# Kernel optimization log

Measured on AMD Instinct MI355X. Metric: run time of the kernel, lower is better.

## Reference

```python
import jax, jax.numpy as jnp
import numpy as np

DIM = 256
HID = 1024
BATCH = 16384
STEP_SIZE = 0.1
NSTEPS = 10  # int(1.0 / step_size)


def setup_inputs() -> dict:
    key = jax.random.key(0)
    ks = jax.random.split(key, 8)
    x = jax.random.normal(ks[0], (BATCH, DIM), dtype=jnp.float32)
    # Scaled init so tanh layers stay in a sane range (like default torch init).
    W1 = jax.random.normal(ks[1], (DIM + 1, HID), dtype=jnp.float32) / np.sqrt(DIM + 1)
    b1 = jnp.zeros((HID,), dtype=jnp.float32)
    W2 = jax.random.normal(ks[2], (HID, HID), dtype=jnp.float32) / np.sqrt(HID)
    b2 = jnp.zeros((HID,), dtype=jnp.float32)
    W3 = jax.random.normal(ks[3], (HID, DIM), dtype=jnp.float32) / np.sqrt(HID)
    b3 = jnp.zeros((DIM,), dtype=jnp.float32)
    proj_mat = jax.random.normal(ks[4], (DIM, DIM), dtype=jnp.float32)
    return {"x": x, "W1": W1, "b1": b1, "W2": W2, "b2": b2,
            "W3": W3, "b3": b3, "proj_mat": proj_mat}


def reference(x, W1, b1, W2, b2, W3, b3, proj_mat):
    """FlowProposal.log_prob: backward RK4 integration of dx/dt = v(x,t)
    from t=1 to t=0 with Hutchinson trace estimation via forward-mode JVP.
    Returns log q(x), shape [batch]."""
    dtype = x.dtype

    def net(xc, t):
        # VelocityMLP: concat(x, t) -> tanh MLP -> velocity [B, DIM]
        tcol = jnp.broadcast_to(jnp.asarray(t, dtype), (xc.shape[0], 1))
        h = jnp.tanh(jnp.concatenate([xc, tcol], axis=1) @ W1 + b1)
        h = jnp.tanh(h @ W2 + b2)
        return h @ W3 + b3

    # Deterministic hashed Hutchinson noise (from the INITIAL x, as in torch).
    noise = jnp.sin((x @ proj_mat) * 1000.0) * 1.41421356  # sqrt(2)

    def dyn(xc, t):
        v, jv = jax.jvp(lambda xi: net(xi, t), (xc,), (noise,))
        tr = jnp.sum(noise * jv, axis=1, keepdims=True)  # eps^T J eps, [B,1]
        return v, tr

    dt = -STEP_SIZE

    def step(carry, k):
        xt, ljt = carry
        t = 1.0 + dt * k
        v1, tr1 = dyn(xt, t)
        v2, tr2 = dyn(xt + dt * 0.5 * v1, t + dt * 0.5)
        v3, tr3 = dyn(xt + dt * 0.5 * v2, t + dt * 0.5)
        v4, tr4 = dyn(xt + dt * v3, t + dt)
        xt = xt + (dt / 6.0) * (v1 + 2 * v2 + 2 * v3 + v4)
        ljt = ljt + (dt / 6.0) * (tr1 + 2 * tr2 + 2 * tr3 + tr4)
        return (xt, ljt), None

    init = (x, jnp.zeros((x.shape[0], 1), dtype))
    (xt, ljt), _ = jax.lax.scan(step, init, jnp.arange(NSTEPS, dtype=dtype))

    log_prob_z = -0.5 * jnp.sum(xt * xt, axis=1) - 0.5 * DIM * jnp.log(jnp.asarray(2.0 * np.pi, dtype))
    return log_prob_z - ljt[:, 0]
```

## Files before the change

### kernel.cpp

```cpp
#include <hip/hip_runtime.h>
#include <stdint.h>
#include <stddef.h>

typedef unsigned short ushort_t;
typedef float f32x4 __attribute__((ext_vector_type(4)));
typedef short short8 __attribute__((ext_vector_type(8)));

#define NB 16384
#define DIMX 256
#define HIDX 1024
#define DTC (-0.1f)

__device__ __forceinline__ unsigned short f2bf_bits(float f){
  unsigned int u = __float_as_uint(f);
  unsigned int r = (u + 0x7FFFu + ((u >> 16) & 1u)) >> 16;
  return (unsigned short)r;
}
__device__ __forceinline__ float bf2f_bits(unsigned short s){
  return __uint_as_float(((unsigned int)s) << 16);
}
__device__ __forceinline__ float fast_tanh(float x){
  float a = fabsf(x);
  float e = __expf(a + a);
  float r = 1.0f - 2.0f / (e + 1.0f);
  return copysignf(r, x);
}
__device__ __forceinline__ void gload16(const void* g, void* l){
  __builtin_amdgcn_global_load_lds(
      (const __attribute__((address_space(1))) void*)g,
      (__attribute__((address_space(3))) void*)l, 16, 0, 0);
}
__device__ __forceinline__ int ldsx(int r, int c){
  return r * 64 + (c ^ ((r & 7) << 3));
}

__global__ void prep_weights(const float* __restrict__ W1, const float* __restrict__ W2,
                             const float* __restrict__ W3,
                             ushort_t* __restrict__ W1at, ushort_t* __restrict__ W2t,
                             ushort_t* __restrict__ W3t){
  int i = blockIdx.x * blockDim.x + threadIdx.x;
  const int T1 = 1024 * 256, T2 = 1024 * 1024, T3 = 256 * 1024;
  if (i < T1){
    int n = i >> 8, k = i & 255;
    W1at[i] = f2bf_bits(W1[k * 1024 + n]);
  } else if (i < T1 + T2){
    int j = i - T1; int n = j >> 10, k = j & 1023;
    W2t[j] = f2bf_bits(W2[k * 1024 + n]);
  } else if (i < T1 + T2 + T3){
    int j = i - T1 - T2; int n = j >> 10, k = j & 1023;
    W3t[j] = f2bf_bits(W3[k * 256 + n]);
  }
}

__global__ void noise_init(const float* __restrict__ x, const float* __restrict__ proj,
                           float* __restrict__ noise_f, ushort_t* __restrict__ noise_bf,
                           float* __restrict__ xt, ushort_t* __restrict__ xcbf,
                           float* __restrict__ ljt){
  const int r0 = blockIdx.x * 8;
  const int j = threadIdx.x;
  __shared__ float xrow[8][256];
  #pragma unroll
  for (int r = 0; r < 8; ++r) xrow[r][j] = x[(size_t)(r0 + r) * 256 + j];
  __syncthreads();
  float s[8] = {0.f,0.f,0.f,0.f,0.f,0.f,0.f,0.f};
  for (int k = 0; k < 256; ++k){
    float p = proj[k * 256 + j];
    #pragma unroll
    for (int r = 0; r < 8; ++r) s[r] = fmaf(xrow[r][k], p, s[r]);
  }
  #pragma unroll
  for (int r = 0; r < 8; ++r){
    float nz = sinf(s[r] * 1000.0f) * 1.41421356237f;
    size_t idx = (size_t)(r0 + r) * 256 + j;
    noise_f[idx] = nz;
    noise_bf[idx] = f2bf_bits(nz);
    float xv = xrow[r][j];
    xt[idx] = xv;
    xcbf[idx] = f2bf_bits(xv);
  }
  if (j < 8) ljt[r0 + j] = 0.0f;
}

template<int BM, int BN, int WGM, int K, int DUAL, int EPI>
__launch_bounds__(512, 2)
__global__ void gemm_kernel(const ushort_t* __restrict__ A1, const ushort_t* __restrict__ A2,
                            const ushort_t* __restrict__ Wt,
                            ushort_t* __restrict__ out1, ushort_t* __restrict__ out2,
                            const float* __restrict__ bias, const float* __restrict__ w1trow,
                            float tval,
                            const ushort_t* __restrict__ dz1,
                            float* __restrict__ xt, float* __restrict__ vacc,
                            ushort_t* __restrict__ xcbf, const float* __restrict__ noise_f,
                            float* __restrict__ ljt, float wdt6, int stage){
  constexpr int BK = 64;
  constexpr int WGN = 8 / WGM;
  constexpr int WM = BM / WGM, WN = BN / WGN;
  constexpr int M_REP = WM / 16, N_REP = WN / 16;
  constexpr int ATILES = DUAL ? 2 : 1;
  constexpr int CH_A = BM / 8;
  constexpr int CH_TOT = ATILES * CH_A + BN / 8;
  constexpr int CH_PW = CH_TOT / 8;

  __shared__ __align__(16) ushort_t lds[(ATILES * BM + BN) * BK];
  ushort_t* ldsA1 = lds;
  ushort_t* ldsA2 = lds + BM * BK;
  ushort_t* ldsB  = lds + ATILES * BM * BK;

  const int m0 = blockIdx.x * BM;
  const int n0 = blockIdx.y * BN;
  const int tid = threadIdx.x;
  const int lane = tid & 63;
  const int wid = tid >> 6;
  const int wr = wid / WGN;
  const int wc = wid % WGN;

  f32x4 acc1[M_REP][N_REP] = {};
  f32x4 acc2[M_REP][N_REP] = {};

  const int srow = lane >> 3;
  const int scol = ((lane & 7) ^ srow) * 8;

  for (int ks = 0; ks < K / BK; ++ks){
    const int k0 = ks * BK;
    #pragma unroll
    for (int c = 0; c < CH_PW; ++c){
      const int ch = wid * CH_PW + c;
      const ushort_t* src;
      if (ch < CH_A){
        src = A1 + (size_t)(m0 + ch * 8 + srow) * K + k0 + scol;
      } else if (DUAL && ch < 2 * CH_A){
        src = A2 + (size_t)(m0 + (ch - CH_A) * 8 + srow) * K + k0 + scol;
      } else {
        src = Wt + (size_t)(n0 + (ch - ATILES * CH_A) * 8 + srow) * K + k0 + scol;
      }
      gload16(src, lds + ch * 512);
    }
    __syncthreads();
    #pragma unroll
    for (int kk = 0; kk < 2; ++kk){
      short8 a1f[M_REP], a2f[M_REP], bfr[N_REP];
      const int lco = kk * 32 + (lane >> 4) * 8;
      const int lro = lane & 15;
      #pragma unroll
      for (int m = 0; m < M_REP; ++m){
        int r = wr * WM + m * 16 + lro;
        a1f[m] = *(const short8*)(ldsA1 + ldsx(r, lco));
        if (DUAL) a2f[m] = *(const short8*)(ldsA2 + ldsx(r, lco));
      }
      #pragma unroll
      for (int n = 0; n < N_REP; ++n){
        int cN = wc * WN + n * 16 + lro;
        bfr[n] = *(const short8*)(ldsB + ldsx(cN, lco));
      }
      #pragma unroll
      for (int m = 0; m < M_REP; ++m){
        #pragma unroll
        for (int n = 0; n < N_REP; ++n){
          acc1[m][n] = __builtin_amdgcn_mfma_f32_16x16x32_bf16(a1f[m], bfr[n], acc1[m][n], 0, 0, 0);
          if (DUAL)
            acc2[m][n] = __builtin_amdgcn_mfma_f32_16x16x32_bf16(a2f[m], bfr[n], acc2[m][n], 0, 0, 0);
        }
      }
    }
    __syncthreads();
  }

  const int rbase = (lane >> 4) * 4;
  const int cbase = lane & 15;
  if (EPI <= 2){
    #pragma unroll
    for (int m = 0; m < M_REP; ++m){
      #pragma unroll
      for (int n = 0; n < N_REP; ++n){
        #pragma unroll
        for (int j = 0; j < 4; ++j){
          const int R = m0 + wr * WM + m * 16 + rbase + j;
          const int C = n0 + wc * WN + n * 16 + cbase;
          const size_t idx = (size_t)R * HIDX + C;
          float a = acc1[m][n][j];
          if (EPI == 0){
            out1[idx] = f2bf_bits(a);
          } else if (EPI == 1){
            float z = a + bias[C] + tval * w1trow[C];
            float h = fast_tanh(z);
            out1[idx] = f2bf_bits(h);
            float d = bf2f_bits(dz1[idx]);
            out2[idx] = f2bf_bits((1.0f - h * h) * d);
          } else {
            float h = fast_tanh(a + bias[C]);
            out1[idx] = f2bf_bits(h);
            out2[idx] = f2bf_bits((1.0f - h * h) * acc2[m][n][j]);
          }
        }
      }
    }
  } else {
    #pragma unroll
    for (int m = 0; m < M_REP; ++m){
      #pragma unroll
      for (int j = 0; j < 4; ++j){
        const int R = m0 + wr * WM + m * 16 + rbase + j;
        float psum = 0.0f;
        #pragma unroll
        for (int n = 0; n < N_REP; ++n){
          const int C = n0 + wc * WN + n * 16 + cbase;
          const size_t idx = (size_t)R * DIMX + C;
          float v = acc1[m][n][j] + bias[C];
          float xtv = xt[idx];
          if (stage == 0){
            vacc[idx] = v;
            xcbf[idx] = f2bf_bits(xtv + 0.5f * DTC * v);
          } else if (stage == 1){
            vacc[idx] += 2.0f * v;
            xcbf[idx] = f2bf_bits(xtv + 0.5f * DTC * v);
          } else if (stage == 2){
            vacc[idx] += 2.0f * v;
            xcbf[idx] = f2bf_bits(xtv + DTC * v);
          } else {
            float xtn = xtv + (DTC / 6.0f) * (vacc[idx] + v);
            xt[idx] = xtn;
            xcbf[idx] = f2bf_bits(xtn);
          }
          psum += noise_f[idx] * acc2[m][n][j];
        }
        #pragma unroll
        for (int off = 1; off < 16; off <<= 1) psum += __shfl_xor(psum, off, 64);
        if (cbase == 0) atomicAdd(&ljt[R], wdt6 * psum);
      }
    }
  }
}

__global__ void final_kernel(const float* __restrict__ xt, const float* __restrict__ ljt,
                             float* __restrict__ out){
  const int row = blockIdx.x * 4 + (threadIdx.x >> 6);
  const int lane = threadIdx.x & 63;
  const float4 xv = *(const float4*)(xt + (size_t)row * 256 + lane * 4);
  float s = xv.x * xv.x + xv.y * xv.y + xv.z * xv.z + xv.w * xv.w;
  #pragma unroll
  for (int off = 32; off; off >>= 1) s += __shfl_xor(s, off, 64);
  if (lane == 0) out[row] = -0.5f * s - 235.2482645f - ljt[row];
}

extern "C" void kernel_launch(void* const* d_in, const int* in_sizes, int n_in,
                              void* d_out, int out_size, void* d_ws, size_t ws_size,
                              hipStream_t stream){
  (void)in_sizes; (void)n_in; (void)out_size; (void)ws_size;
  const float* x    = (const float*)d_in[0];
  const float* W1   = (const float*)d_in[1];
  const float* b1   = (const float*)d_in[2];
  const float* W2   = (const float*)d_in[3];
  const float* b2   = (const float*)d_in[4];
  const float* W3   = (const float*)d_in[5];
  const float* b3   = (const float*)d_in[6];
  const float* proj = (const float*)d_in[7];

  size_t off = 0;
  char* wsb = (char*)d_ws;
  auto carve = [&](size_t n) -> char* {
    char* p = wsb + off; off += (n + 255) & ~(size_t)255; return p;
  };
  ushort_t* W1at     = (ushort_t*)carve((size_t)1024 * 256 * 2);
  ushort_t* W2t      = (ushort_t*)carve((size_t)1024 * 1024 * 2);
  ushort_t* W3t      = (ushort_t*)carve((size_t)256 * 1024 * 2);
  float*    noise_f  = (float*)carve((size_t)NB * 256 * 4);
  ushort_t* noise_bf = (ushort_t*)carve((size_t)NB * 256 * 2);
  ushort_t* dz1      = (ushort_t*)carve((size_t)NB * 1024 * 2);
  float*    xt       = (float*)carve((size_t)NB * 256 * 4);
  ushort_t* xcbf     = (ushort_t*)carve((size_t)NB * 256 * 2);
  float*    vacc     = (float*)carve((size_t)NB * 256 * 4);
  float*    ljt      = (float*)carve((size_t)NB * 4);
  ushort_t* h1       = (ushort_t*)carve((size_t)NB * 1024 * 2);
  ushort_t* dh1      = (ushort_t*)carve((size_t)NB * 1024 * 2);
  ushort_t* h2       = (ushort_t*)carve((size_t)NB * 1024 * 2);
  ushort_t* dh2      = (ushort_t*)carve((size_t)NB * 1024 * 2);

  prep_weights<<<6144, 256, 0, stream>>>(W1, W2, W3, W1at, W2t, W3t);
  noise_init<<<NB / 8, 256, 0, stream>>>(x, proj, noise_f, noise_bf, xt, xcbf, ljt);

  gemm_kernel<256, 256, 2, 256, 0, 0><<<dim3(NB / 256, 4), 512, 0, stream>>>(
      noise_bf, nullptr, W1at, dz1, nullptr, nullptr, nullptr, 0.f, nullptr,
      nullptr, nullptr, nullptr, nullptr, nullptr, 0.f, 0);

  const float toff[4] = {0.0f, -0.05f, -0.05f, -0.1f};
  const float wst[4]  = {1.0f, 2.0f, 2.0f, 1.0f};
  for (int k = 0; k < 10; ++k){
    float t = 1.0f - 0.1f * (float)k;
    for (int s = 0; s < 4; ++s){
      gemm_kernel<256, 256, 2, 256, 0, 1><<<dim3(NB / 256, 4), 512, 0, stream>>>(
          xcbf, nullptr, W1at, h1, dh1, b1, W1 + 256 * 1024, t + toff[s], dz1,
          nullptr, nullptr, nullptr, nullptr, nullptr, 0.f, 0);
      gemm_kernel<128, 256, 2, 1024, 1, 2><<<dim3(NB / 128, 4), 512, 0, stream>>>(
          h1, dh1, W2t, h2, dh2, b2, nullptr, 0.f, nullptr,
          nullptr, nullptr, nullptr, nullptr, nullptr, 0.f, 0);
      gemm_kernel<128, 128, 4, 1024, 1, 3><<<dim3(NB / 128, 2), 512, 0, stream>>>(
          h2, dh2, W3t, nullptr, nullptr, b3, nullptr, 0.f, nullptr,
          xt, vacc, xcbf, noise_f, ljt, wst[s] * (DTC / 6.0f), s);
    }
  }
  final_kernel<<<NB / 4, 256, 0, stream>>>(xt, ljt, (float*)d_out);
}
```

Before: 6.728 ms.

## Double-buffer GEMM LDS tiles with async loads and vmcnt-based waits

Replaces the single-buffered K loop, which loaded, synchronised, computed and synchronised again, with a two-stage ping-pong LDS pipeline. The next K-tile is issued through global_load_lds while the current tile is being computed, and explicit s_waitcnt vmcnt plus s_barrier replace __syncthreads. Per-chunk source pointers are hoisted out of the loop. The aim is to hide global-memory latency behind MFMA work, at the cost of twice the shared memory per block, which may reduce occupancy.

```diff
diff --git a/kernel.cpp b/kernel.cpp
--- a/kernel.cpp
+++ b/kernel.cpp
@@ -29,6 +29,15 @@
   __builtin_amdgcn_global_load_lds(
       (const __attribute__((address_space(1))) void*)g,
       (__attribute__((address_space(3))) void*)l, 16, 0, 0);
+}
+template<int N> __device__ __forceinline__ void wait_vmcnt(){
+  if constexpr (N == 0)      asm volatile("s_waitcnt vmcnt(0)" ::: "memory");
+  else if constexpr (N == 4) asm volatile("s_waitcnt vmcnt(4)" ::: "memory");
+  else if constexpr (N == 6) asm volatile("s_waitcnt vmcnt(6)" ::: "memory");
+  else if constexpr (N == 8) asm volatile("s_waitcnt vmcnt(8)" ::: "memory");
+  else if constexpr (N == 12) asm volatile("s_waitcnt vmcnt(12)" ::: "memory");
+  else if constexpr (N == 16) asm volatile("s_waitcnt vmcnt(16)" ::: "memory");
+  else static_assert(N == 0, "unsupported vmcnt");
 }
 __device__ __forceinline__ int ldsx(int r, int c){
   return r * 64 + (c ^ ((r & 7) << 3));
@@ -91,7 +100,7 @@
                             const ushort_t* __restrict__ dz1,
                             float* __restrict__ xt, float* __restrict__ vacc,
                             ushort_t* __restrict__ xcbf, const float* __restrict__ noise_f,
-                            float* __restrict__ ljt, float wdt6, int stage){
+                            float* __restrict__ ljt, float wdt6, int rk){
   constexpr int BK = 64;
   constexpr int WGN = 8 / WGM;
   constexpr int WM = BM / WGM, WN = BN / WGN;
@@ -100,11 +109,11 @@
   constexpr int CH_A = BM / 8;
   constexpr int CH_TOT = ATILES * CH_A + BN / 8;
   constexpr int CH_PW = CH_TOT / 8;
-
-  __shared__ __align__(16) ushort_t lds[(ATILES * BM + BN) * BK];
-  ushort_t* ldsA1 = lds;
-  ushort_t* ldsA2 = lds + BM * BK;
-  ushort_t* ldsB  = lds + ATILES * BM * BK;
+  constexpr int BUF_E = (ATILES * BM + BN) * BK;
+  constexpr int NK = K / BK;
+  static_assert(NK >= 2, "pipeline needs >=2 K-steps");
+
+  __shared__ __align__(16) ushort_t lds[2 * BUF_E];
 
   const int m0 = blockIdx.x * BM;
   const int n0 = blockIdx.y * BN;
@@ -120,22 +129,30 @@
   const int srow = lane >> 3;
   const int scol = ((lane & 7) ^ srow) * 8;
 
-  for (int ks = 0; ks < K / BK; ++ks){
+  const ushort_t* srcb[CH_PW];
+  #pragma unroll
+  for (int c = 0; c < CH_PW; ++c){
+    const int ch = wid * CH_PW + c;
+    if (ch < CH_A)
+      srcb[c] = A1 + (size_t)(m0 + ch * 8 + srow) * K + scol;
+    else if (DUAL && ch < 2 * CH_A)
+      srcb[c] = A2 + (size_t)(m0 + (ch - CH_A) * 8 + srow) * K + scol;
+    else
+      srcb[c] = Wt + (size_t)(n0 + (ch - ATILES * CH_A) * 8 + srow) * K + scol;
+  }
+
+  auto do_stage = [&](int buf, int ks){
+    ushort_t* dst = lds + buf * BUF_E + (wid * CH_PW) * 512;
     const int k0 = ks * BK;
     #pragma unroll
-    for (int c = 0; c < CH_PW; ++c){
-      const int ch = wid * CH_PW + c;
-      const ushort_t* src;
-      if (ch < CH_A){
-        src = A1 + (size_t)(m0 + ch * 8 + srow) * K + k0 + scol;
-      } else if (DUAL && ch < 2 * CH_A){
-        src = A2 + (size_t)(m0 + (ch - CH_A) * 8 + srow) * K + k0 + scol;
-      } else {
-        src = Wt + (size_t)(n0 + (ch - ATILES * CH_A) * 8 + srow) * K + k0 + scol;
-      }
-      gload16(src, lds + ch * 512);
-    }
-    __syncthreads();
+    for (int c = 0; c < CH_PW; ++c)
+      gload16(srcb[c] + k0, dst + c * 512);
+  };
+
+  auto compute = [&](int buf){
+    const ushort_t* ldsA1 = lds + buf * BUF_E;
+    const ushort_t* ldsA2 = ldsA1 + BM * BK;
+    const ushort_t* ldsB  = ldsA1 + ATILES * BM * BK;
     #pragma unroll
     for (int kk = 0; kk < 2; ++kk){
       short8 a1f[M_REP], a2f[M_REP], bfr[N_REP];
@@ -162,8 +179,23 @@
         }
       }
     }
-    __syncthreads();
-  }
+  };
+
+  do_stage(0, 0);
+  do_stage(1, 1);
+  for (int ks = 0; ks < NK - 2; ++ks){
+    wait_vmcnt<CH_PW>();
+    __builtin_amdgcn_s_barrier();
+    compute(ks & 1);
+    __builtin_amdgcn_s_barrier();
+    do_stage(ks & 1, ks + 2);
+  }
+  wait_vmcnt<CH_PW>();
+  __builtin_amdgcn_s_barrier();
+  compute(NK & 1);
+  wait_vmcnt<0>();
+  __builtin_amdgcn_s_barrier();
+  compute((NK - 1) & 1);
 
   const int rbase = (lane >> 4) * 4;
   const int cbase = lane & 15;
@@ -207,13 +239,13 @@
           const size_t idx = (size_t)R * DIMX + C;
           float v = acc1[m][n][j] + bias[C];
           float xtv = xt[idx];
-          if (stage == 0){
+          if (rk == 0){
             vacc[idx] = v;
             xcbf[idx] = f2bf_bits(xtv + 0.5f * DTC * v);
-          } else if (stage == 1){
+          } else if (rk == 1){
             vacc[idx] += 2.0f * v;
             xcbf[idx] = f2bf_bits(xtv + 0.5f * DTC * v);
-          } else if (stage == 2){
+          } else if (rk == 2){
             vacc[idx] += 2.0f * v;
             xcbf[idx] = f2bf_bits(xtv + DTC * v);
           } else {
```

After: 7.777 ms. 1.16x slower.
